# Kernel tuning notes

Measured on AMD Instinct MI355X. Metric: run time of the kernel, lower is better.

## Reference

```python
import jax, jax.numpy as jnp
import numpy as np

LEVELS = [(128, 128), (64, 64), (32, 32), (16, 16)]  # (H_l, W_l) per feature level
N_TOTAL = sum(h * w for h, w in LEVELS)  # 21760
B, D, H, P, L = 2, 256, 8, 4, 4
HD = D // H
FFN_DIM = 1024


def setup_inputs() -> dict:
    key = jax.random.key(0)
    ks = jax.random.split(key, 12)
    s = 0.02  # weight init scale
    return {
        'embed': jax.random.normal(ks[0], (B, N_TOTAL, D), jnp.float32),
        'pos': jax.random.normal(ks[1], (B, N_TOTAL, D), jnp.float32),
        'ref_points': jax.random.uniform(ks[2], (B, N_TOTAL, L, 2), jnp.float32),
        'ln1_w': jnp.ones((D,), jnp.float32), 'ln1_b': jnp.zeros((D,), jnp.float32),
        'ln2_w': jnp.ones((D,), jnp.float32), 'ln2_b': jnp.zeros((D,), jnp.float32),
        'Wv': jax.random.normal(ks[3], (D, D), jnp.float32) * s, 'bv': jnp.zeros((D,), jnp.float32),
        'Woff': jax.random.normal(ks[4], (D, H * L * P * 2), jnp.float32) * s, 'boff': jnp.zeros((H * L * P * 2,), jnp.float32),
        'Wattn': jax.random.normal(ks[5], (D, H * L * P), jnp.float32) * s, 'battn': jnp.zeros((H * L * P,), jnp.float32),
        'Wo': jax.random.normal(ks[6], (D, D), jnp.float32) * s, 'bo': jnp.zeros((D,), jnp.float32),
        'W1': jax.random.normal(ks[7], (D, FFN_DIM), jnp.float32) * s, 'b1': jnp.zeros((FFN_DIM,), jnp.float32),
        'W2': jax.random.normal(ks[8], (FFN_DIM, D), jnp.float32) * s, 'b2': jnp.zeros((D,), jnp.float32),
        'dimensions': jnp.array(LEVELS, jnp.int32),
    }


def _layer_norm(x, w, b):
    m = jnp.mean(x, axis=-1, keepdims=True)
    v = jnp.mean(jnp.square(x - m), axis=-1, keepdims=True)
    return (x - m) * jax.lax.rsqrt(v + 1e-5) * w + b


def _msda(q, ref, v, dims, Wv, bv, Woff, boff, Wattn, battn, Wo, bo):
    # q, v: (B, N, D); ref: (B, N, L, 2) normalized (x, y)
    Bq, N, _ = q.shape
    value = (v @ Wv + bv).reshape(Bq, N, H, HD)
    off = (q @ Woff + boff).reshape(Bq, N, H, L, P, 2)
    aw = jax.nn.softmax((q @ Wattn + battn).reshape(Bq, N, H, L * P), axis=-1)
    aw = aw.reshape(Bq, N, H, L, P)
    # offset normalizer is [W_l, H_l]
    norm = jnp.stack([dims[:, 1], dims[:, 0]], axis=-1).astype(q.dtype)  # (L, 2)
    loc = ref[:, :, None, :, None, :] + off / norm[None, None, None, :, None, :]  # (B,N,H,L,P,2)

    out = jnp.zeros((Bq, N, H, HD), q.dtype)
    start = 0
    for l, (Hl, Wl) in enumerate(LEVELS):
        S = Hl * Wl
        vl = value[:, start:start + S].transpose(0, 2, 1, 3)  # (B, H, S, hd)
        start += S
        # grid_sample semantics: align_corners=False, zero padding
        x = loc[:, :, :, l, :, 0] * Wl - 0.5  # (B, N, H, P)
        y = loc[:, :, :, l, :, 1] * Hl - 0.5
        x0 = jnp.floor(x); y0 = jnp.floor(y)
        wx = x - x0; wy = y - y0
        x0i = x0.astype(jnp.int32); y0i = y0.astype(jnp.int32)
        samp = jnp.zeros(x.shape + (HD,), q.dtype)
        for dy, dx, w in ((0, 0, (1 - wx) * (1 - wy)), (0, 1, wx * (1 - wy)),
                          (1, 0, (1 - wx) * wy), (1, 1, wx * wy)):
            xi = x0i + dx; yi = y0i + dy
            valid = (xi >= 0) & (xi < Wl) & (yi >= 0) & (yi < Hl)
            idx = jnp.clip(yi, 0, Hl - 1) * Wl + jnp.clip(xi, 0, Wl - 1)  # (B, N, H, P)
            idx_t = idx.transpose(0, 2, 1, 3).reshape(Bq, H, N * P)
            g = jnp.take_along_axis(vl, idx_t[..., None], axis=2)  # (B, H, N*P, hd)
            g = g.reshape(Bq, H, N, P, HD).transpose(0, 2, 1, 3, 4)  # (B, N, H, P, hd)
            samp = samp + (w * valid)[..., None] * g
        out = out + jnp.sum(samp * aw[:, :, :, l, :, None], axis=3)
    return out.reshape(Bq, N, D) @ Wo + bo


def reference(embed, pos, ref_points, ln1_w, ln1_b, ln2_w, ln2_b, Wv, bv, Woff, boff,
              Wattn, battn, Wo, bo, W1, b1, W2, b2, dimensions):
    v = _layer_norm(embed, ln1_w, ln1_b)
    q = v + pos
    embed = embed + _msda(q, ref_points, v, dimensions, Wv, bv, Woff, boff, Wattn, battn, Wo, bo)
    f = _layer_norm(embed, ln2_w, ln2_b)
    embed = embed + jax.nn.relu(f @ W1 + b1) @ W2 + b2
    return embed
```

## Files before the change

kernel.cpp:

```cpp
#include <hip/hip_runtime.h>
#include <cstdint>
#include <cstddef>

#define N_TOTAL 21760
#define BATCH   2
#define M_TOT   (BATCH * N_TOTAL)
#define DMODEL  256
#define NHEAD   8
#define HDIM    32
#define FFN     1024

typedef __bf16 b16x8 __attribute__((ext_vector_type(8)));
typedef float  f32x4 __attribute__((ext_vector_type(4)));

__device__ __forceinline__ unsigned short f2b(float f) {
  union { float f; unsigned u; } v; v.f = f;
  unsigned r = v.u + 0x7FFF + ((v.u >> 16) & 1);
  return (unsigned short)(r >> 16);
}
__device__ __forceinline__ float b2f(unsigned short u) {
  union { unsigned u; float f; } v; v.u = (unsigned)u << 16;
  return v.f;
}

__global__ void wconv_all(const float* __restrict__ Wv, const float* __restrict__ Woff,
                          const float* __restrict__ Wattn, const float* __restrict__ Wo,
                          const float* __restrict__ W1, const float* __restrict__ W2,
                          unsigned short* __restrict__ dstbase) {
  int idx = blockIdx.x * 256 + threadIdx.x;
  const float* src; int K, N, off;
  if (idx < 65536)       { src = Wv;    K = 256;  N = 256;  off = 0;      }
  else if (idx < 131072) { src = Woff;  K = 256;  N = 256;  off = 65536;  idx -= 65536; }
  else if (idx < 163840) { src = Wattn; K = 256;  N = 128;  off = 131072; idx -= 131072; }
  else if (idx < 229376) { src = Wo;    K = 256;  N = 256;  off = 163840; idx -= 163840; }
  else if (idx < 491520) { src = W1;    K = 256;  N = 1024; off = 229376; idx -= 229376; }
  else if (idx < 753664) { src = W2;    K = 1024; N = 256;  off = 491520; idx -= 491520; }
  else return;
  int k = idx / N, n = idx - k * N;
  dstbase[off + (size_t)n * K + k] = f2b(src[idx]);
}

__global__ void ln1_kernel(const float* __restrict__ x, const float* __restrict__ pos,
                           const float* __restrict__ w, const float* __restrict__ b,
                           unsigned short* __restrict__ vb, unsigned short* __restrict__ qb) {
  int t = threadIdx.x;
  int tkn = blockIdx.x * 4 + (t >> 6);
  int lane = t & 63;
  size_t base = (size_t)tkn * DMODEL + lane * 4;
  float4 xv = *(const float4*)&x[base];
  float s1 = xv.x + xv.y + xv.z + xv.w;
  float s2 = xv.x * xv.x + xv.y * xv.y + xv.z * xv.z + xv.w * xv.w;
  #pragma unroll
  for (int off = 32; off; off >>= 1) {
    s1 += __shfl_down(s1, off);
    s2 += __shfl_down(s2, off);
  }
  s1 = __shfl(s1, 0); s2 = __shfl(s2, 0);
  float m   = s1 * (1.0f / DMODEL);
  float var = s2 * (1.0f / DMODEL) - m * m;
  float rs  = rsqrtf(var + 1e-5f);
  float4 wv = *(const float4*)&w[lane * 4];
  float4 bv = *(const float4*)&b[lane * 4];
  float4 pv = *(const float4*)&pos[base];
  float o0 = (xv.x - m) * rs * wv.x + bv.x;
  float o1 = (xv.y - m) * rs * wv.y + bv.y;
  float o2 = (xv.z - m) * rs * wv.z + bv.z;
  float o3 = (xv.w - m) * rs * wv.w + bv.w;
  ushort4 vo = {f2b(o0), f2b(o1), f2b(o2), f2b(o3)};
  ushort4 qo = {f2b(o0 + pv.x), f2b(o1 + pv.y), f2b(o2 + pv.z), f2b(o3 + pv.w)};
  *(ushort4*)&vb[base] = vo;
  *(ushort4*)&qb[base] = qo;
}

__global__ void ln2_kernel(const float* __restrict__ x, const float* __restrict__ w,
                           const float* __restrict__ b, unsigned short* __restrict__ yb) {
  int t = threadIdx.x;
  int tkn = blockIdx.x * 4 + (t >> 6);
  int lane = t & 63;
  size_t base = (size_t)tkn * DMODEL + lane * 4;
  float4 xv = *(const float4*)&x[base];
  float s1 = xv.x + xv.y + xv.z + xv.w;
  float s2 = xv.x * xv.x + xv.y * xv.y + xv.z * xv.z + xv.w * xv.w;
  #pragma unroll
  for (int off = 32; off; off >>= 1) {
    s1 += __shfl_down(s1, off);
    s2 += __shfl_down(s2, off);
  }
  s1 = __shfl(s1, 0); s2 = __shfl(s2, 0);
  float m   = s1 * (1.0f / DMODEL);
  float var = s2 * (1.0f / DMODEL) - m * m;
  float rs  = rsqrtf(var + 1e-5f);
  float4 wv = *(const float4*)&w[lane * 4];
  float4 bv = *(const float4*)&b[lane * 4];
  ushort4 vo = {f2b((xv.x - m) * rs * wv.x + bv.x), f2b((xv.y - m) * rs * wv.y + bv.y),
                f2b((xv.z - m) * rs * wv.z + bv.z), f2b((xv.w - m) * rs * wv.w + bv.w)};
  *(ushort4*)&yb[base] = vo;
}

__global__ void gemm_bf16(const unsigned short* __restrict__ A,
                          const unsigned short* __restrict__ Bt,
                          const float* __restrict__ bias, const float* __restrict__ addsrc,
                          float* __restrict__ Cf, unsigned short* __restrict__ Cb,
                          int K, int N, int relu) {
  __shared__ unsigned short As[128 * 72];
  __shared__ unsigned short Bs[128 * 72];
  int t    = threadIdx.x;
  int row0 = blockIdx.x * 128;
  int col0 = blockIdx.y * 128;
  int w    = t >> 6;
  int l    = t & 63;
  int wm   = w >> 1, wn = w & 1;
  int lr   = l & 15;
  int kq   = l >> 4;

  f32x4 acc[4][4];
  #pragma unroll
  for (int i = 0; i < 4; ++i)
    #pragma unroll
    for (int j = 0; j < 4; ++j) acc[i][j] = (f32x4){0.f, 0.f, 0.f, 0.f};

  for (int k0 = 0; k0 < K; k0 += 64) {
    #pragma unroll
    for (int i = 0; i < 4; ++i) {
      int c = i * 256 + t;
      int row = c >> 3, seg = c & 7;
      float4 va = *(const float4*)&A [(size_t)(row0 + row) * K + k0 + seg * 8];
      float4 vb = *(const float4*)&Bt[(size_t)(col0 + row) * K + k0 + seg * 8];
      *(float4*)&As[row * 72 + seg * 8] = va;
      *(float4*)&Bs[row * 72 + seg * 8] = vb;
    }
    __syncthreads();
    #pragma unroll
    for (int kk = 0; kk < 2; ++kk) {
      b16x8 aF[4], bF[4];
      #pragma unroll
      for (int i = 0; i < 4; ++i)
        aF[i] = *(const b16x8*)&As[(wm * 64 + i * 16 + lr) * 72 + kk * 32 + kq * 8];
      #pragma unroll
      for (int j = 0; j < 4; ++j)
        bF[j] = *(const b16x8*)&Bs[(wn * 64 + j * 16 + lr) * 72 + kk * 32 + kq * 8];
      #pragma unroll
      for (int i = 0; i < 4; ++i)
        #pragma unroll
        for (int j = 0; j < 4; ++j)
          acc[i][j] = __builtin_amdgcn_mfma_f32_16x16x32_bf16(aF[i], bF[j], acc[i][j], 0, 0, 0);
    }
    __syncthreads();
  }

  #pragma unroll
  for (int j = 0; j < 4; ++j) {
    int colg = col0 + wn * 64 + j * 16 + lr;
    float bcol = bias[colg];
    #pragma unroll
    for (int i = 0; i < 4; ++i) {
      int r0g = row0 + wm * 64 + i * 16 + kq * 4;
      #pragma unroll
      for (int r = 0; r < 4; ++r) {
        int rowg = r0g + r;
        float o = acc[i][j][r] + bcol;
        if (relu) o = fmaxf(o, 0.0f);
        if (addsrc) o += addsrc[(size_t)rowg * N + colg];
        if (Cf) Cf[(size_t)rowg * N + colg] = o;
        if (Cb) Cb[(size_t)rowg * N + colg] = f2b(o);
      }
    }
  }
}

__global__ void msda_kernel(const unsigned short* __restrict__ value,
                            const unsigned short* __restrict__ offb,
                            const unsigned short* __restrict__ awb,
                            const float* __restrict__ ref,
                            unsigned short* __restrict__ outb) {
  __shared__ int2 P[512];
  int tkn = blockIdx.x;
  int t   = threadIdx.x;
  int b   = (tkn >= N_TOTAL) ? 1 : 0;

  if (t < 128) {
    int h = t >> 4, s = t & 15, lev = s >> 2, p = s & 3;
    float lg = b2f(awb[(size_t)tkn * 128 + h * 16 + s]);
    float mx = lg;
    #pragma unroll
    for (int m = 1; m < 16; m <<= 1) mx = fmaxf(mx, __shfl_xor(mx, m, 16));
    float e = __expf(lg - mx);
    float sum = e;
    #pragma unroll
    for (int m = 1; m < 16; m <<= 1) sum += __shfl_xor(sum, m, 16);
    float aw = e / sum;

    const int HL[4] = {128, 64, 32, 16};
    const int ST[4] = {0, 16384, 20480, 21504};
    int Wl = HL[lev];
    float rx = ref[(size_t)tkn * 8 + lev * 2 + 0];
    float ry = ref[(size_t)tkn * 8 + lev * 2 + 1];
    float ox = b2f(offb[(size_t)tkn * 256 + h * 32 + lev * 8 + p * 2 + 0]);
    float oy = b2f(offb[(size_t)tkn * 256 + h * 32 + lev * 8 + p * 2 + 1]);
    float x = rx * (float)Wl + ox - 0.5f;
    float y = ry * (float)Wl + oy - 0.5f;
    float x0f = floorf(x), y0f = floorf(y);
    float wx = x - x0f, wy = y - y0f;
    int x0 = (int)x0f, y0 = (int)y0f;
    float wt[4] = {(1.f - wx) * (1.f - wy), wx * (1.f - wy),
                   (1.f - wx) * wy, wx * wy};
    int base = b * N_TOTAL + ST[lev];
    #pragma unroll
    for (int tp = 0; tp < 4; ++tp) {
      int xi = x0 + (tp & 1), yi = y0 + (tp >> 1);
      bool ok = (xi >= 0) & (xi < Wl) & (yi >= 0) & (yi < Wl);
      float wgt = ok ? aw * wt[tp] : 0.f;
      int boff  = ok ? (((base + yi * Wl + xi) * 256 + h * 32) * 2) : 0;
      P[t * 4 + tp] = (int2){__float_as_int(wgt), boff};
    }
  }
  __syncthreads();

  int h = t >> 5, g = t & 31, dp = g & 15, half = g >> 4;
  int o = h * 64 + half * 32;
  int doff = dp * 4;
  const char* vbase = (const char*)value;
  float accL = 0.f, accH = 0.f;
  #pragma unroll 8
  for (int j = 0; j < 32; ++j) {
    int2 pr = P[o + j];
    float wgt = __int_as_float(pr.x);
    unsigned v = *(const unsigned*)(vbase + (size_t)(unsigned)pr.y + doff);
    union { unsigned u; float f; } lo, hi;
    lo.u = v << 16;
    hi.u = v & 0xffff0000u;
    accL += wgt * lo.f;
    accH += wgt * hi.f;
  }
  accL += __shfl_xor(accL, 16);
  accH += __shfl_xor(accH, 16);
  if (half == 0) {
    unsigned pk = (unsigned)f2b(accL) | ((unsigned)f2b(accH) << 16);
    *(unsigned*)&outb[(size_t)tkn * 256 + h * 32 + dp * 2] = pk;
  }
}

extern "C" void kernel_launch(void* const* d_in, const int* in_sizes, int n_in,
                              void* d_out, int out_size, void* d_ws, size_t ws_size,
                              hipStream_t stream) {
  const float* embed = (const float*)d_in[0];
  const float* pos   = (const float*)d_in[1];
  const float* refp  = (const float*)d_in[2];
  const float* ln1w  = (const float*)d_in[3];
  const float* ln1b  = (const float*)d_in[4];
  const float* ln2w  = (const float*)d_in[5];
  const float* ln2b  = (const float*)d_in[6];
  const float* Wv    = (const float*)d_in[7];
  const float* bv    = (const float*)d_in[8];
  const float* Woff  = (const float*)d_in[9];
  const float* boff  = (const float*)d_in[10];
  const float* Wattn = (const float*)d_in[11];
  const float* battn = (const float*)d_in[12];
  const float* Wo    = (const float*)d_in[13];
  const float* bo    = (const float*)d_in[14];
  const float* W1    = (const float*)d_in[15];
  const float* b1    = (const float*)d_in[16];
  const float* W2    = (const float*)d_in[17];
  const float* b2    = (const float*)d_in[18];
  float* out = (float*)d_out;
  float* ws  = (float*)d_ws;

  const size_t U = (size_t)M_TOT * DMODEL;
  unsigned short* valb16 = (unsigned short*)ws;
  unsigned short* offb16 = (unsigned short*)(ws + U / 2);
  unsigned short* awb16  = (unsigned short*)(ws + U);
  unsigned short* msdab  = (unsigned short*)(ws + U + U / 4);
  unsigned short* hid16  = (unsigned short*)ws;
  float*          embed2 = ws + 2 * U;
  unsigned short* vb16   = (unsigned short*)(ws + 3 * U);
  unsigned short* qb16   = (unsigned short*)(ws + 3 * U + U / 2);
  unsigned short* fb16   = (unsigned short*)(ws + 4 * U);
  unsigned short* wbuf   = (unsigned short*)(ws + 4 * U + U / 2);

  unsigned short* Wvt    = wbuf;
  unsigned short* Wofft  = wbuf + 65536;
  unsigned short* Wattnt = wbuf + 131072;
  unsigned short* Wot    = wbuf + 163840;
  unsigned short* W1t    = wbuf + 229376;
  unsigned short* W2t    = wbuf + 491520;

  wconv_all<<<(753664 + 255) / 256, 256, 0, stream>>>(Wv, Woff, Wattn, Wo, W1, W2, wbuf);

  ln1_kernel<<<M_TOT / 4, 256, 0, stream>>>(embed, pos, ln1w, ln1b, vb16, qb16);

  gemm_bf16<<<dim3(M_TOT / 128, 2), 256, 0, stream>>>(
      vb16, Wvt, bv, nullptr, nullptr, valb16, 256, 256, 0);
  gemm_bf16<<<dim3(M_TOT / 128, 2), 256, 0, stream>>>(
      qb16, Wofft, boff, nullptr, nullptr, offb16, 256, 256, 0);
  gemm_bf16<<<dim3(M_TOT / 128, 1), 256, 0, stream>>>(
      qb16, Wattnt, battn, nullptr, nullptr, awb16, 256, 128, 0);

  msda_kernel<<<M_TOT, 256, 0, stream>>>(valb16, offb16, awb16, refp, msdab);

  gemm_bf16<<<dim3(M_TOT / 128, 2), 256, 0, stream>>>(
      msdab, Wot, bo, embed, embed2, nullptr, 256, 256, 0);

  ln2_kernel<<<M_TOT / 4, 256, 0, stream>>>(embed2, ln2w, ln2b, fb16);

  gemm_bf16<<<dim3(M_TOT / 128, 8), 256, 0, stream>>>(
      fb16, W1t, b1, nullptr, nullptr, hid16, 256, 1024, 1);
  gemm_bf16<<<dim3(M_TOT / 128, 2), 256, 0, stream>>>(
      hid16, W2t, b2, embed2, out, nullptr, 1024, 256, 0);
}
```

Measured before the change: 354.2 us.

## Prefetch GEMM tiles in registers, merge projection GEMMs, widen MSDA gathers

The GEMM core now loads the next K-tile from global memory into registers while MFMAs run on the current shared-memory tile, so load latency overlaps compute. The three projection GEMMs (value, offset, attention logits) are merged into one launch with five column groups, which cuts launch overhead and fills the GPU better. The MSDA kernel now has each thread gather 8-byte chunks for 16 samples, using a padded shared-memory layout to avoid bank conflicts, and reduces across lanes with two shuffles. The register prefetch raises register pressure and may lower occupancy.

```diff
diff --git a/kernel.cpp b/kernel.cpp
--- a/kernel.cpp
+++ b/kernel.cpp
@@ -97,21 +97,19 @@
   *(ushort4*)&yb[base] = vo;
 }
 
-__global__ void gemm_bf16(const unsigned short* __restrict__ A,
-                          const unsigned short* __restrict__ Bt,
-                          const float* __restrict__ bias, const float* __restrict__ addsrc,
-                          float* __restrict__ Cf, unsigned short* __restrict__ Cb,
-                          int K, int N, int relu) {
-  __shared__ unsigned short As[128 * 72];
-  __shared__ unsigned short Bs[128 * 72];
-  int t    = threadIdx.x;
-  int row0 = blockIdx.x * 128;
-  int col0 = blockIdx.y * 128;
-  int w    = t >> 6;
-  int l    = t & 63;
-  int wm   = w >> 1, wn = w & 1;
-  int lr   = l & 15;
-  int kq   = l >> 4;
+__device__ __forceinline__ void gemm_core(
+    const unsigned short* __restrict__ A, const unsigned short* __restrict__ Bt,
+    const float* __restrict__ bias, const float* __restrict__ addsrc,
+    float* __restrict__ Cf, unsigned short* __restrict__ Cb,
+    int K, int N, int relu, int row0, int col0,
+    unsigned short* As, unsigned short* Bs) {
+  int t  = threadIdx.x;
+  int w  = t >> 6;
+  int l  = t & 63;
+  int wm = w >> 1, wn = w & 1;
+  int lr = l & 15;
+  int kq = l >> 4;
+  int srow = t >> 3, sseg = t & 7;
 
   f32x4 acc[4][4];
   #pragma unroll
@@ -119,17 +117,30 @@
     #pragma unroll
     for (int j = 0; j < 4; ++j) acc[i][j] = (f32x4){0.f, 0.f, 0.f, 0.f};
 
+  float4 pa[4], pb[4];
+  #pragma unroll
+  for (int i = 0; i < 4; ++i) {
+    int c = i * 256 + t; int row = c >> 3, seg = c & 7;
+    pa[i] = *(const float4*)&A [(size_t)(row0 + row) * K + seg * 8];
+    pb[i] = *(const float4*)&Bt[(size_t)(col0 + row) * K + seg * 8];
+  }
+
   for (int k0 = 0; k0 < K; k0 += 64) {
     #pragma unroll
     for (int i = 0; i < 4; ++i) {
-      int c = i * 256 + t;
-      int row = c >> 3, seg = c & 7;
-      float4 va = *(const float4*)&A [(size_t)(row0 + row) * K + k0 + seg * 8];
-      float4 vb = *(const float4*)&Bt[(size_t)(col0 + row) * K + k0 + seg * 8];
-      *(float4*)&As[row * 72 + seg * 8] = va;
-      *(float4*)&Bs[row * 72 + seg * 8] = vb;
+      int c = i * 256 + t; int row = c >> 3, seg = c & 7;
+      *(float4*)&As[row * 72 + seg * 8] = pa[i];
+      *(float4*)&Bs[row * 72 + seg * 8] = pb[i];
     }
     __syncthreads();
+    if (k0 + 64 < K) {
+      #pragma unroll
+      for (int i = 0; i < 4; ++i) {
+        int c = i * 256 + t; int row = c >> 3, seg = c & 7;
+        pa[i] = *(const float4*)&A [(size_t)(row0 + row) * K + k0 + 64 + seg * 8];
+        pb[i] = *(const float4*)&Bt[(size_t)(col0 + row) * K + k0 + 64 + seg * 8];
+      }
+    }
     #pragma unroll
     for (int kk = 0; kk < 2; ++kk) {
       b16x8 aF[4], bF[4];
@@ -168,12 +179,45 @@
   }
 }
 
+__global__ void gemm_bf16(const unsigned short* __restrict__ A,
+                          const unsigned short* __restrict__ Bt,
+                          const float* __restrict__ bias, const float* __restrict__ addsrc,
+                          float* __restrict__ Cf, unsigned short* __restrict__ Cb,
+                          int K, int N, int relu) {
+  __shared__ unsigned short As[128 * 72];
+  __shared__ unsigned short Bs[128 * 72];
+  gemm_core(A, Bt, bias, addsrc, Cf, Cb, K, N, relu,
+            blockIdx.x * 128, blockIdx.y * 128, As, Bs);
+}
+
+__global__ void gemm_proj(const unsigned short* __restrict__ vb,
+                          const unsigned short* __restrict__ qb,
+                          const unsigned short* __restrict__ Wvt,
+                          const unsigned short* __restrict__ Wofft,
+                          const unsigned short* __restrict__ Wattnt,
+                          const float* __restrict__ bv, const float* __restrict__ boff,
+                          const float* __restrict__ battn,
+                          unsigned short* __restrict__ valb,
+                          unsigned short* __restrict__ offb,
+                          unsigned short* __restrict__ awb) {
+  __shared__ unsigned short As[128 * 72];
+  __shared__ unsigned short Bs[128 * 72];
+  int y = blockIdx.y;
+  const unsigned short* A; const unsigned short* Bt; const float* bias;
+  unsigned short* C; int col0, N;
+  if (y < 2)      { A = vb; Bt = Wvt;    bias = bv;    C = valb; col0 = y * 128;       N = 256; }
+  else if (y < 4) { A = qb; Bt = Wofft;  bias = boff;  C = offb; col0 = (y - 2) * 128; N = 256; }
+  else            { A = qb; Bt = Wattnt; bias = battn; C = awb;  col0 = 0;             N = 128; }
+  gemm_core(A, Bt, bias, nullptr, nullptr, C, 256, N, 0,
+            blockIdx.x * 128, col0, As, Bs);
+}
+
 __global__ void msda_kernel(const unsigned short* __restrict__ value,
                             const unsigned short* __restrict__ offb,
                             const unsigned short* __restrict__ awb,
                             const float* __restrict__ ref,
                             unsigned short* __restrict__ outb) {
-  __shared__ int2 P[512];
+  __shared__ int2 P[552];
   int tkn = blockIdx.x;
   int t   = threadIdx.x;
   int b   = (tkn >= N_TOTAL) ? 1 : 0;
@@ -205,38 +249,44 @@
     float wt[4] = {(1.f - wx) * (1.f - wy), wx * (1.f - wy),
                    (1.f - wx) * wy, wx * wy};
     int base = b * N_TOTAL + ST[lev];
+    int pbase = h * 68 + (s >> 2) * 17 + (s & 3) * 4;
     #pragma unroll
     for (int tp = 0; tp < 4; ++tp) {
       int xi = x0 + (tp & 1), yi = y0 + (tp >> 1);
       bool ok = (xi >= 0) & (xi < Wl) & (yi >= 0) & (yi < Wl);
       float wgt = ok ? aw * wt[tp] : 0.f;
-      int boff  = ok ? (((base + yi * Wl + xi) * 256 + h * 32) * 2) : 0;
-      P[t * 4 + tp] = (int2){__float_as_int(wgt), boff};
+      int boff2 = ok ? (((base + yi * Wl + xi) * 256 + h * 32) * 2) : 0;
+      P[pbase + tp] = (int2){__float_as_int(wgt), boff2};
     }
   }
   __syncthreads();
 
-  int h = t >> 5, g = t & 31, dp = g & 15, half = g >> 4;
-  int o = h * 64 + half * 32;
-  int doff = dp * 4;
+  int h = t >> 5, q = (t >> 3) & 3, dq = t & 7;
+  int o = h * 68 + q * 17;
+  unsigned doff = dq * 8;
   const char* vbase = (const char*)value;
-  float accL = 0.f, accH = 0.f;
+  float a0 = 0.f, a1 = 0.f, a2 = 0.f, a3 = 0.f;
   #pragma unroll 8
-  for (int j = 0; j < 32; ++j) {
+  for (int j = 0; j < 16; ++j) {
     int2 pr = P[o + j];
     float wgt = __int_as_float(pr.x);
-    unsigned v = *(const unsigned*)(vbase + (size_t)(unsigned)pr.y + doff);
-    union { unsigned u; float f; } lo, hi;
-    lo.u = v << 16;
-    hi.u = v & 0xffff0000u;
-    accL += wgt * lo.f;
-    accH += wgt * hi.f;
-  }
-  accL += __shfl_xor(accL, 16);
-  accH += __shfl_xor(accH, 16);
-  if (half == 0) {
-    unsigned pk = (unsigned)f2b(accL) | ((unsigned)f2b(accH) << 16);
-    *(unsigned*)&outb[(size_t)tkn * 256 + h * 32 + dp * 2] = pk;
+    unsigned off = (unsigned)pr.y + doff;
+    uint2 v = *(const uint2*)(vbase + off);
+    union { unsigned u; float f; } l0, h0, l1, h1;
+    l0.u = v.x << 16; h0.u = v.x & 0xffff0000u;
+    l1.u = v.y << 16; h1.u = v.y & 0xffff0000u;
+    a0 += wgt * l0.f; a1 += wgt * h0.f;
+    a2 += wgt * l1.f; a3 += wgt * h1.f;
+  }
+  a0 += __shfl_xor(a0, 8);  a1 += __shfl_xor(a1, 8);
+  a2 += __shfl_xor(a2, 8);  a3 += __shfl_xor(a3, 8);
+  a0 += __shfl_xor(a0, 16); a1 += __shfl_xor(a1, 16);
+  a2 += __shfl_xor(a2, 16); a3 += __shfl_xor(a3, 16);
+  if (q == 0) {
+    uint2 pk;
+    pk.x = (unsigned)f2b(a0) | ((unsigned)f2b(a1) << 16);
+    pk.y = (unsigned)f2b(a2) | ((unsigned)f2b(a3) << 16);
+    *(uint2*)&outb[(size_t)tkn * 256 + h * 32 + dq * 4] = pk;
   }
 }
 
@@ -288,12 +338,8 @@
 
   ln1_kernel<<<M_TOT / 4, 256, 0, stream>>>(embed, pos, ln1w, ln1b, vb16, qb16);
 
-  gemm_bf16<<<dim3(M_TOT / 128, 2), 256, 0, stream>>>(
-      vb16, Wvt, bv, nullptr, nullptr, valb16, 256, 256, 0);
-  gemm_bf16<<<dim3(M_TOT / 128, 2), 256, 0, stream>>>(
-      qb16, Wofft, boff, nullptr, nullptr, offb16, 256, 256, 0);
-  gemm_bf16<<<dim3(M_TOT / 128, 1), 256, 0, stream>>>(
-      qb16, Wattnt, battn, nullptr, nullptr, awb16, 256, 128, 0);
+  gemm_proj<<<dim3(M_TOT / 128, 5), 256, 0, stream>>>(
+      vb16, qb16, Wvt, Wofft, Wattnt, bv, boff, battn, valb16, offb16, awb16);
 
   msda_kernel<<<M_TOT, 256, 0, stream>>>(valb16, offb16, awb16, refp, msdab);
 
```

Result: slower. 669.5 us (+89.0%).
